# Optimization experiments

Hardware: AMD Instinct MI355X
Metric: run time of the kernel (lower is better)

## Reference

```python
import jax, jax.numpy as jnp
import numpy as np

B, J, K, M, D = 64, 8, 64, 32, 256
TEMP = 0.1
EPS = 1e-8  # torch CosineSimilarity eps
NUM_LABELS = 16


def setup_inputs() -> dict:
    key = jax.random.key(0)
    k1, k2, k3, k4, k5 = jax.random.split(key, 5)
    return {
        "childrens": jax.random.normal(k1, (B, J, D), jnp.float32),
        "childrens_pos": jax.random.normal(k2, (B, J, D), jnp.float32),
        "childrens_negs": jax.random.normal(k3, (B, K, M, D), jnp.float32),
        "childrens_gt_labels": jax.random.randint(k4, (B, J), 0, NUM_LABELS),
        "childrens_gt_label_negs": jax.random.randint(k5, (B, K, M), 0, NUM_LABELS),
    }


def _cos(a, b):
    # cosine similarity over last axis with torch-style eps clamping
    na = jnp.maximum(jnp.linalg.norm(a, axis=-1), EPS)
    nb = jnp.maximum(jnp.linalg.norm(b, axis=-1), EPS)
    return jnp.sum(a * b, axis=-1) / (na * nb)


def reference(childrens, childrens_pos, childrens_negs, childrens_gt_labels, childrens_gt_label_negs):
    # Faithful to the original indentation bug: only the LAST child (j = J-1)
    # of each group i contributes to the loss.
    Bn = childrens.shape[0]
    child = childrens[:, -1]                    # [B, D]
    pos = childrens_pos[:, -1]                  # [B, D]
    label = childrens_gt_labels[:, -1]          # [B]

    negs = childrens_negs.reshape(Bn, -1, childrens_negs.shape[-1])   # [B, K*M, D]
    neg_labels = childrens_gt_label_negs.reshape(Bn, -1)              # [B, K*M]

    pos_sim = _cos(child, pos) / TEMP                                 # [B]
    neg_sim = _cos(child[:, None, :], negs) / TEMP                    # [B, K*M]

    # Only negatives whose gt label equals the child's label are included;
    # excluded ones get -inf so they vanish from the CE partition function.
    mask = neg_labels == label[:, None]
    neg_sim = jnp.where(mask, neg_sim, -jnp.inf)

    logits = jnp.concatenate([pos_sim[:, None], neg_sim], axis=1)     # [B, 1+K*M]
    # CrossEntropyLoss(reduction='sum') with target class 0
    loss = jax.nn.logsumexp(logits, axis=1) - pos_sim                 # [B]
    return jnp.sum(loss) / (2 * Bn)
```

## Files before the change

### kernel.cpp

```cpp
#include <hip/hip_runtime.h>
#include <math.h>

constexpr int B = 64, J = 8, K = 64, M = 32, D = 256;
constexpr int NNEG = K * M;
constexpr float TEMP = 0.1f;
constexpr float EPS = 1e-8f;
constexpr float SHIFT = 10.0f;

constexpr int SLICES = 8;
constexpr int NEG_PER_BLOCK = NNEG / SLICES;
constexpr int NBLK = B * SLICES;

__global__ __launch_bounds__(256) void neg_partial_kernel(
    const float* __restrict__ childrens,
    const float* __restrict__ childrens_pos,
    const int*   __restrict__ gt_labels,
    const float* __restrict__ negs,
    const int*   __restrict__ neg_labels,
    float*       __restrict__ partials,
    float*       __restrict__ pos_sims) {
  const int blk  = blockIdx.x;
  const int b    = blk >> 3;
  const int s    = blk & 7;
  const int tid  = threadIdx.x;
  const int lane = tid & 63;
  const int wave = tid >> 6;

  const float* child = childrens + ((size_t)b * J + (J - 1)) * D;
  const float4 cv = ((const float4*)child)[lane];
  const int label = gt_labels[b * J + (J - 1)];
  const int neg_base = s * NEG_PER_BLOCK + wave * 64;
  const int nlab = neg_labels[(size_t)b * NNEG + neg_base + lane];

  float4 pv = make_float4(0.f, 0.f, 0.f, 0.f);
  const bool do_pos = (s == 0) && (wave == 0);
  if (do_pos)
    pv = ((const float4*)(childrens_pos + ((size_t)b * J + (J - 1)) * D))[lane];

  float ss = cv.x * cv.x + cv.y * cv.y + cv.z * cv.z + cv.w * cv.w;
  #pragma unroll
  for (int off = 32; off > 0; off >>= 1) ss += __shfl_down(ss, off, 64);
  const float cn_inv_t = 1.0f / (fmaxf(sqrtf(ss), EPS) * TEMP);

  const float* nv_base = negs + (size_t)b * NNEG * D;
  unsigned long long mask = __ballot(nlab == label);

  float acc = 0.0f;
  while (mask) {
    int idx[8];
    int cnt = 1;
    idx[0] = __ffsll((long long)mask) - 1;
    mask &= mask - 1;
    #pragma unroll
    for (int t = 1; t < 8; ++t) {
      if (mask) {
        idx[t] = __ffsll((long long)mask) - 1;
        mask &= mask - 1;
        ++cnt;
      } else {
        idx[t] = idx[0];
      }
    }

    float dot[8], nn[8];
    #pragma unroll
    for (int t = 0; t < 8; ++t) {
      const float4 x =
          ((const float4*)(nv_base + (size_t)(neg_base + idx[t]) * D))[lane];
      dot[t] = cv.x * x.x + cv.y * x.y + cv.z * x.z + cv.w * x.w;
      nn[t]  = x.x * x.x + x.y * x.y + x.z * x.z + x.w * x.w;
    }
    #pragma unroll
    for (int off = 32; off > 0; off >>= 1) {
      #pragma unroll
      for (int t = 0; t < 8; ++t) {
        dot[t] += __shfl_down(dot[t], off, 64);
        nn[t]  += __shfl_down(nn[t],  off, 64);
      }
    }
    if (lane == 0) {
      #pragma unroll
      for (int t = 0; t < 8; ++t) {
        if (t < cnt) {
          const float sim = dot[t] * cn_inv_t / fmaxf(sqrtf(nn[t]), EPS);
          acc += expf(sim - SHIFT);
        }
      }
    }
  }

  if (do_pos) {
    float pp = pv.x * pv.x + pv.y * pv.y + pv.z * pv.z + pv.w * pv.w;
    float cp = cv.x * pv.x + cv.y * pv.y + cv.z * pv.z + cv.w * pv.w;
    #pragma unroll
    for (int off = 32; off > 0; off >>= 1) {
      pp += __shfl_down(pp, off, 64);
      cp += __shfl_down(cp, off, 64);
    }
    if (lane == 0) {
      const float pos_sim = cp * cn_inv_t / fmaxf(sqrtf(pp), EPS);
      pos_sims[b] = pos_sim;
      acc += expf(pos_sim - SHIFT);
    }
  }

  if (lane == 0) partials[blk * 4 + wave] = acc;
}

__global__ __launch_bounds__(64) void finalize_kernel(
    const float* __restrict__ partials,
    const float* __restrict__ pos_sims,
    float*       __restrict__ out) {
  const int lane = threadIdx.x;
  float sum = 0.0f;
  #pragma unroll
  for (int t = 0; t < SLICES * 4; ++t) sum += partials[lane * SLICES * 4 + t];
  const float ps = pos_sims[lane];
  float loss = logf(sum) + SHIFT - ps;
  #pragma unroll
  for (int off = 32; off > 0; off >>= 1) loss += __shfl_down(loss, off, 64);
  if (lane == 0) out[0] = loss / (2.0f * B);
}

extern "C" void kernel_launch(void* const* d_in, const int* in_sizes, int n_in,
                              void* d_out, int out_size, void* d_ws, size_t ws_size,
                              hipStream_t stream) {
  const float* childrens      = (const float*)d_in[0];
  const float* childrens_pos  = (const float*)d_in[1];
  const float* childrens_negs = (const float*)d_in[2];
  const int*   gt_labels      = (const int*)d_in[3];
  const int*   gt_label_negs  = (const int*)d_in[4];
  float* out = (float*)d_out;

  float* partials = (float*)d_ws;
  float* pos_sims = partials + NBLK * 4;

  neg_partial_kernel<<<NBLK, 256, 0, stream>>>(
      childrens, childrens_pos, gt_labels, childrens_negs, gt_label_negs,
      partials, pos_sims);
  finalize_kernel<<<1, 64, 0, stream>>>(partials, pos_sims, out);
}
```

Baseline: 176.3 us.

## Split each wave into four 16-lane groups processing separate negatives

Restructures the per-wave dot-product work so that each 16-lane group handles its own negative vector, with each lane loading four float4 chunks. Every wave-wide 6-step shuffle reduction for eight negatives becomes a 4-step xor reduction within the group, cutting cross-lane shuffle traffic and instruction count. Partial sums are combined across groups at the end. The finalize kernel also switches to float4 loads. The cost is more registers per lane for the child and negative vectors.

```diff
diff --git a/kernel.cpp b/kernel.cpp
--- a/kernel.cpp
+++ b/kernel.cpp
@@ -25,21 +25,33 @@
   const int tid  = threadIdx.x;
   const int lane = tid & 63;
   const int wave = tid >> 6;
+  const int g    = lane >> 4;
+  const int gl   = lane & 15;
 
   const float* child = childrens + ((size_t)b * J + (J - 1)) * D;
-  const float4 cv = ((const float4*)child)[lane];
+  float4 cv[4];
+  #pragma unroll
+  for (int q = 0; q < 4; ++q) cv[q] = ((const float4*)child)[gl + 16 * q];
+
   const int label = gt_labels[b * J + (J - 1)];
   const int neg_base = s * NEG_PER_BLOCK + wave * 64;
   const int nlab = neg_labels[(size_t)b * NNEG + neg_base + lane];
 
-  float4 pv = make_float4(0.f, 0.f, 0.f, 0.f);
   const bool do_pos = (s == 0) && (wave == 0);
-  if (do_pos)
-    pv = ((const float4*)(childrens_pos + ((size_t)b * J + (J - 1)) * D))[lane];
+  float4 pv[4] = {make_float4(0.f,0.f,0.f,0.f), make_float4(0.f,0.f,0.f,0.f),
+                  make_float4(0.f,0.f,0.f,0.f), make_float4(0.f,0.f,0.f,0.f)};
+  if (do_pos) {
+    const float* posp = childrens_pos + ((size_t)b * J + (J - 1)) * D;
+    #pragma unroll
+    for (int q = 0; q < 4; ++q) pv[q] = ((const float4*)posp)[gl + 16 * q];
+  }
 
-  float ss = cv.x * cv.x + cv.y * cv.y + cv.z * cv.z + cv.w * cv.w;
+  float ss = 0.f;
   #pragma unroll
-  for (int off = 32; off > 0; off >>= 1) ss += __shfl_down(ss, off, 64);
+  for (int q = 0; q < 4; ++q)
+    ss += cv[q].x*cv[q].x + cv[q].y*cv[q].y + cv[q].z*cv[q].z + cv[q].w*cv[q].w;
+  #pragma unroll
+  for (int off = 8; off > 0; off >>= 1) ss += __shfl_xor(ss, off, 64);
   const float cn_inv_t = 1.0f / (fmaxf(sqrtf(ss), EPS) * TEMP);
 
   const float* nv_base = negs + (size_t)b * NNEG * D;
@@ -62,40 +74,56 @@
       }
     }
 
-    float dot[8], nn[8];
+    const int my0 = (g == 0) ? idx[0] : (g == 1) ? idx[1] : (g == 2) ? idx[2] : idx[3];
+    const int my1 = (g == 0) ? idx[4] : (g == 1) ? idx[5] : (g == 2) ? idx[6] : idx[7];
+
+    const float* p0 = nv_base + (size_t)(neg_base + my0) * D;
+    const float* p1 = nv_base + (size_t)(neg_base + my1) * D;
+
+    float4 x0[4], x1[4];
     #pragma unroll
-    for (int t = 0; t < 8; ++t) {
-      const float4 x =
-          ((const float4*)(nv_base + (size_t)(neg_base + idx[t]) * D))[lane];
-      dot[t] = cv.x * x.x + cv.y * x.y + cv.z * x.z + cv.w * x.w;
-      nn[t]  = x.x * x.x + x.y * x.y + x.z * x.z + x.w * x.w;
+    for (int q = 0; q < 4; ++q) {
+      x0[q] = ((const float4*)p0)[gl + 16 * q];
+      x1[q] = ((const float4*)p1)[gl + 16 * q];
+    }
+
+    float dot0 = 0.f, nn0 = 0.f, dot1 = 0.f, nn1 = 0.f;
+    #pragma unroll
+    for (int q = 0; q < 4; ++q) {
+      dot0 += cv[q].x*x0[q].x + cv[q].y*x0[q].y + cv[q].z*x0[q].z + cv[q].w*x0[q].w;
+      nn0  += x0[q].x*x0[q].x + x0[q].y*x0[q].y + x0[q].z*x0[q].z + x0[q].w*x0[q].w;
+      dot1 += cv[q].x*x1[q].x + cv[q].y*x1[q].y + cv[q].z*x1[q].z + cv[q].w*x1[q].w;
+      nn1  += x1[q].x*x1[q].x + x1[q].y*x1[q].y + x1[q].z*x1[q].z + x1[q].w*x1[q].w;
     }
     #pragma unroll
-    for (int off = 32; off > 0; off >>= 1) {
-      #pragma unroll
-      for (int t = 0; t < 8; ++t) {
-        dot[t] += __shfl_down(dot[t], off, 64);
-        nn[t]  += __shfl_down(nn[t],  off, 64);
-      }
+    for (int off = 8; off > 0; off >>= 1) {
+      dot0 += __shfl_xor(dot0, off, 64);
+      nn0  += __shfl_xor(nn0,  off, 64);
+      dot1 += __shfl_xor(dot1, off, 64);
+      nn1  += __shfl_xor(nn1,  off, 64);
     }
-    if (lane == 0) {
-      #pragma unroll
-      for (int t = 0; t < 8; ++t) {
-        if (t < cnt) {
-          const float sim = dot[t] * cn_inv_t / fmaxf(sqrtf(nn[t]), EPS);
-          acc += expf(sim - SHIFT);
-        }
-      }
+    if (gl == 0) {
+      if (g < cnt)
+        acc += expf(dot0 * cn_inv_t / fmaxf(sqrtf(nn0), EPS) - SHIFT);
+      if (4 + g < cnt)
+        acc += expf(dot1 * cn_inv_t / fmaxf(sqrtf(nn1), EPS) - SHIFT);
     }
   }
 
+  acc += __shfl_xor(acc, 16, 64);
+  acc += __shfl_xor(acc, 32, 64);
+
   if (do_pos) {
-    float pp = pv.x * pv.x + pv.y * pv.y + pv.z * pv.z + pv.w * pv.w;
-    float cp = cv.x * pv.x + cv.y * pv.y + cv.z * pv.z + cv.w * pv.w;
+    float pp = 0.f, cp = 0.f;
     #pragma unroll
-    for (int off = 32; off > 0; off >>= 1) {
-      pp += __shfl_down(pp, off, 64);
-      cp += __shfl_down(cp, off, 64);
+    for (int q = 0; q < 4; ++q) {
+      pp += pv[q].x*pv[q].x + pv[q].y*pv[q].y + pv[q].z*pv[q].z + pv[q].w*pv[q].w;
+      cp += cv[q].x*pv[q].x + cv[q].y*pv[q].y + cv[q].z*pv[q].z + cv[q].w*pv[q].w;
+    }
+    #pragma unroll
+    for (int off = 8; off > 0; off >>= 1) {
+      pp += __shfl_xor(pp, off, 64);
+      cp += __shfl_xor(cp, off, 64);
     }
     if (lane == 0) {
       const float pos_sim = cp * cn_inv_t / fmaxf(sqrtf(pp), EPS);
@@ -112,9 +140,13 @@
     const float* __restrict__ pos_sims,
     float*       __restrict__ out) {
   const int lane = threadIdx.x;
+  const float4* p = (const float4*)(partials + (size_t)lane * SLICES * 4);
   float sum = 0.0f;
   #pragma unroll
-  for (int t = 0; t < SLICES * 4; ++t) sum += partials[lane * SLICES * 4 + t];
+  for (int t = 0; t < SLICES; ++t) {
+    const float4 v = p[t];
+    sum += v.x + v.y + v.z + v.w;
+  }
   const float ps = pos_sims[lane];
   float loss = logf(sum) + SHIFT - ps;
   #pragma unroll
```

Measured after the change: 173.8 us. No clear change (-1.5%).
